# Kernel optimization log

Measured on AMD Instinct MI355X. Metric: run time of the kernel, lower is better.

## Reference

```python
import jax, jax.numpy as jnp
import numpy as np

B, D_IN, J = 65536, 512, 8
HIDDEN = [256, 128, 64]


def setup_inputs() -> dict:
    key = jax.random.key(0)
    ks = jax.random.split(key, 8)
    dims = [D_IN] + HIDDEN
    inp = {
        "x": jax.random.normal(ks[0], (B, D_IN), dtype=jnp.float32),
        # soft domain indicator (one-hot in practice; math is a weighted sum either way)
        "domain_indicator": jax.random.uniform(ks[1], (B, J), dtype=jnp.float32),
    }
    for i in range(3):
        fin, fout = dims[i], dims[i + 1]
        scale = (2.0 / (fin + fout)) ** 0.5  # glorot_normal
        inp[f"sk{i}"] = jax.random.normal(ks[2 + i], (fin, fout), dtype=jnp.float32) * scale
        inp[f"sb{i}"] = jnp.zeros((fout,), dtype=jnp.float32)
        inp[f"dk{i}"] = jax.random.normal(ks[5 + i], (J, fin, fout), dtype=jnp.float32) * scale
        inp[f"db{i}"] = jnp.zeros((J, fout), dtype=jnp.float32)
    return inp


def _star_forward(x, domain_indicator, layers):
    # layer 0: x is [B, D]; fused shared*domain weights -> batched per-domain GEMM
    sk, sb, dk, db = layers[0]
    w = sk[None] * dk                                   # [J, D, H0]
    h = jnp.einsum('bi,jio->bjo', x, w) + (sb[None] + db)[None]  # [B, J, H0]
    h = jax.nn.relu(h)
    for sk, sb, dk, db in layers[1:]:
        w = sk[None] * dk                               # [J, Hi, Hi+1]
        h = jnp.einsum('bji,jio->bjo', h, w) + (sb[None] + db)[None]
        h = jax.nn.relu(h)
    # select/mix domains: sum_j h[b,j,:] * indicator[b,j]
    return jnp.einsum('bjo,bj->bo', h, domain_indicator)


def reference(x, domain_indicator, sk0, sb0, dk0, db0, sk1, sb1, dk1, db1, sk2, sb2, dk2, db2):
    layers = [(sk0, sb0, dk0, db0), (sk1, sb1, dk1, db1), (sk2, sb2, dk2, db2)]
    return _star_forward(x, domain_indicator, layers)
```

## Files before the change

### kernel.cpp

```cpp
#include <hip/hip_runtime.h>
#include <stdint.h>


namespace {

typedef __attribute__((ext_vector_type(8))) short bf16x8;
typedef __attribute__((ext_vector_type(4))) float f32x4;

union Frag { bf16x8 v; unsigned int u[4]; };

constexpr size_t WS_L0   = 0;
constexpr size_t WS_L1   = 4194304;
constexpr size_t WS_L2   = 5242880;
constexpr size_t WS_B0   = 5505024;
constexpr size_t WS_B1   = 5513216;
constexpr size_t WS_B2   = 5517312;
constexpr size_t WS_X    = 5519360;
constexpr size_t WS_TOTAL_BIG = WS_X + (size_t)65536 * 2048;

constexpr int PREP_TOTAL = 1048576 + 262144 + 65536 + 2048 + 1024 + 512;

__device__ __forceinline__ void splitpair(float a, float b,
                                          unsigned int& hi, unsigned int& lo) {
    unsigned int ua = __float_as_uint(a);
    unsigned int ub = __float_as_uint(b);
    unsigned int ha = ua & 0xffff0000u;
    unsigned int hb = ub & 0xffff0000u;
    float ra = a - __uint_as_float(ha);
    float rb = b - __uint_as_float(hb);
    hi = (ua >> 16) | hb;
    lo = (__float_as_uint(ra) >> 16) | (__float_as_uint(rb) & 0xffff0000u);
}

__device__ __forceinline__ void split16(float v, unsigned short& h, unsigned short& l) {
    unsigned int u = __float_as_uint(v);
    h = (unsigned short)(u >> 16);
    float r = v - __uint_as_float(u & 0xffff0000u);
    l = (unsigned short)(__float_as_uint(r) >> 16);
}

__device__ __forceinline__ unsigned int packsplit(float v) {
    unsigned int u = __float_as_uint(v);
    unsigned int h = u & 0xffff0000u;
    float r = v - __uint_as_float(h);
    return h | (__float_as_uint(r) >> 16);
}

__device__ __forceinline__ void unpack2(unsigned int e0, unsigned int e1,
                                        unsigned int& hi, unsigned int& lo) {
    hi = (e0 >> 16) | (e1 & 0xffff0000u);
    lo = (e0 & 0xffffu) | (e1 << 16);
}

__global__ void prep_ws(const float* __restrict__ sk0, const float* __restrict__ dk0,
                        const float* __restrict__ sk1, const float* __restrict__ dk1,
                        const float* __restrict__ sk2, const float* __restrict__ dk2,
                        const float* __restrict__ sb0, const float* __restrict__ db0,
                        const float* __restrict__ sb1, const float* __restrict__ db1,
                        const float* __restrict__ sb2, const float* __restrict__ db2,
                        char* __restrict__ ws) {
    int tid = blockIdx.x * 256 + threadIdx.x;
    if (tid < 1048576) {
        int n = tid & 255, k = (tid >> 8) & 511, j = tid >> 17;
        float wv = sk0[k * 256 + n] * dk0[(size_t)(j * 512 + k) * 256 + n];
        unsigned int u = __float_as_uint(wv);
        unsigned int h = u & 0xffff0000u;
        float r = wv - __uint_as_float(h);
        int pair = (j * 16 + (k >> 5)) * 16 + (n >> 4);
        int lane = (n & 15) | (((k >> 3) & 3) << 4);
        size_t off = WS_L0 + (size_t)pair * 2048 + lane * 16 + (k & 7) * 2;
        *(unsigned short*)(ws + off)        = (unsigned short)(u >> 16);
        *(unsigned short*)(ws + off + 1024) = (unsigned short)(__float_as_uint(r) >> 16);
    } else if (tid < 1310720) {
        int t = tid - 1048576;
        int n = t & 127, k = (t >> 7) & 255, j = t >> 15;
        float wv = sk1[k * 128 + n] * dk1[(size_t)(j * 256 + k) * 128 + n];
        unsigned int u = __float_as_uint(wv);
        unsigned int h = u & 0xffff0000u;
        float r = wv - __uint_as_float(h);
        int pair = (j * 8 + (k >> 5)) * 8 + (n >> 4);
        int lane = (n & 15) | (((k >> 3) & 3) << 4);
        size_t off = WS_L1 + (size_t)pair * 2048 + lane * 16 + (k & 7) * 2;
        *(unsigned short*)(ws + off)        = (unsigned short)(u >> 16);
        *(unsigned short*)(ws + off + 1024) = (unsigned short)(__float_as_uint(r) >> 16);
    } else if (tid < 1376256) {
        int t = tid - 1310720;
        int n = t & 63, k = (t >> 6) & 127, j = t >> 13;
        float wv = sk2[k * 64 + n] * dk2[(size_t)(j * 128 + k) * 64 + n];
        unsigned int u = __float_as_uint(wv);
        unsigned int h = u & 0xffff0000u;
        float r = wv - __uint_as_float(h);
        int pair = (j * 4 + (k >> 5)) * 4 + (n >> 4);
        int lane = (n & 15) | (((k >> 3) & 3) << 4);
        size_t off = WS_L2 + (size_t)pair * 2048 + lane * 16 + (k & 7) * 2;
        *(unsigned short*)(ws + off)        = (unsigned short)(u >> 16);
        *(unsigned short*)(ws + off + 1024) = (unsigned short)(__float_as_uint(r) >> 16);
    } else if (tid < 1378304) {
        int t = tid - 1376256;
        ((float*)(ws + WS_B0))[t] = sb0[t & 255] + db0[t];
    } else if (tid < 1379328) {
        int t = tid - 1378304;
        ((float*)(ws + WS_B1))[t] = sb1[t & 127] + db1[t];
    } else if (tid < PREP_TOTAL) {
        int t = tid - 1379328;
        ((float*)(ws + WS_B2))[t] = sb2[t & 63] + db2[t];
    }
}

__global__ __launch_bounds__(256) void prep_xsplit(const float* __restrict__ x,
                                                   char* __restrict__ ws) {
    __shared__ __align__(16) unsigned int xf[8192];
    const int b     = blockIdx.x;
    const int tid   = threadIdx.x;
    const int row16 = tid >> 4;
    const int seg   = tid & 15;

    const float* src = x + ((size_t)b * 16 + row16) * 512 + seg * 32;
    float4 a[8];
#pragma unroll
    for (int i = 0; i < 8; ++i) a[i] = *(const float4*)(src + i * 4);

    unsigned int hi[16], lo[16];
#pragma unroll
    for (int i = 0; i < 8; ++i) {
        splitpair(a[i].x, a[i].y, hi[2 * i],     lo[2 * i]);
        splitpair(a[i].z, a[i].w, hi[2 * i + 1], lo[2 * i + 1]);
    }
#pragma unroll
    for (int qq = 0; qq < 4; ++qq) {
        const int lane = row16 | (qq << 4);
        const int di = seg * 512 + lane * 4;
        uint4 vh = { hi[qq * 4 + 0], hi[qq * 4 + 1], hi[qq * 4 + 2], hi[qq * 4 + 3] };
        uint4 vl = { lo[qq * 4 + 0], lo[qq * 4 + 1], lo[qq * 4 + 2], lo[qq * 4 + 3] };
        *(uint4*)&xf[di]       = vh;
        *(uint4*)&xf[di + 256] = vl;
    }
    __syncthreads();

    uint4* dst = (uint4*)(ws + WS_X + (size_t)b * 32768) + tid * 8;
#pragma unroll
    for (int i = 0; i < 8; ++i) dst[i] = *(const uint4*)&xf[tid * 32 + i * 4];
}

__global__ __launch_bounds__(512, 4) void star_mfma_v5(
    const float* __restrict__ ind,
    const char* __restrict__ ws,
    float* __restrict__ out)
{
    __shared__ __align__(16) unsigned short H0hi[32 * 264];
    __shared__ __align__(16) unsigned short H0lo[32 * 264];
    __shared__ __align__(16) unsigned short H1hi[32 * 136];
    __shared__ __align__(16) unsigned short H1lo[32 * 136];
    __shared__ float indS[8 * 33];

    const int tid  = threadIdx.x;
    const int w    = tid >> 6;
    const int lane = tid & 63;
    const int c    = lane & 15;
    const int q    = lane >> 4;
    const int b0   = blockIdx.x * 32;
    const int mt2  = w >> 2;
    const int nt2  = w & 3;

    const char* xp  = ws + WS_X;
    const char* wB0 = ws + WS_L0;
    const char* wB1 = ws + WS_L1;
    const char* wB2 = ws + WS_L2;
    const float* bias0 = (const float*)(ws + WS_B0);
    const float* bias1 = (const float*)(ws + WS_B1);
    const float* bias2 = (const float*)(ws + WS_B2);

    if (tid < 256) indS[(tid & 7) * 33 + (tid >> 3)] = ind[(size_t)b0 * 8 + tid];

    const f32x4 z = {0.f, 0.f, 0.f, 0.f};
    f32x4 oacc = z;

    __syncthreads();

    for (int jp = 0; jp < 2; ++jp) {
        f32x4 acc0[4][2][2];
#pragma unroll
        for (int jj = 0; jj < 4; ++jj)
#pragma unroll
            for (int mt = 0; mt < 2; ++mt)
#pragma unroll
                for (int ntl = 0; ntl < 2; ++ntl) acc0[jj][mt][ntl] = z;

        for (int kc = 0; kc < 16; ++kc) {
            Frag Ahi[2], Alo[2];
#pragma unroll
            for (int mt = 0; mt < 2; ++mt) {
                const char* ap = xp + ((size_t)((blockIdx.x * 2 + mt) * 16 + kc) * 2048) + lane * 16;
                *(uint4*)Ahi[mt].u = *(const uint4*)ap;
                *(uint4*)Alo[mt].u = *(const uint4*)(ap + 1024);
            }
#pragma unroll
            for (int jj = 0; jj < 4; ++jj) {
                const int j = jp * 4 + jj;
#pragma unroll
                for (int ntl = 0; ntl < 2; ++ntl) {
                    const int nt = w * 2 + ntl;
                    const char* pb = wB0 + ((size_t)((j * 16 + kc) * 16 + nt) * 2048) + lane * 16;
                    Frag Bhi, Blo;
                    *(uint4*)Bhi.u = *(const uint4*)pb;
                    *(uint4*)Blo.u = *(const uint4*)(pb + 1024);
#pragma unroll
                    for (int mt = 0; mt < 2; ++mt) {
                        acc0[jj][mt][ntl] = __builtin_amdgcn_mfma_f32_16x16x32_bf16(Ahi[mt].v, Bhi.v, acc0[jj][mt][ntl], 0, 0, 0);
                        acc0[jj][mt][ntl] = __builtin_amdgcn_mfma_f32_16x16x32_bf16(Ahi[mt].v, Blo.v, acc0[jj][mt][ntl], 0, 0, 0);
                        acc0[jj][mt][ntl] = __builtin_amdgcn_mfma_f32_16x16x32_bf16(Alo[mt].v, Bhi.v, acc0[jj][mt][ntl], 0, 0, 0);
                    }
                }
            }
        }

#pragma unroll
        for (int jj = 0; jj < 4; ++jj) {
            const int j = jp * 4 + jj;

#pragma unroll
            for (int ntl = 0; ntl < 2; ++ntl) {
                const int k = w * 32 + ntl * 16 + c;
                const float bv = bias0[j * 256 + k];
#pragma unroll
                for (int mt = 0; mt < 2; ++mt)
#pragma unroll
                    for (int r = 0; r < 4; ++r) {
                        float v = fmaxf(acc0[jj][mt][ntl][r] + bv, 0.f);
                        unsigned short h16, l16;
                        split16(v, h16, l16);
                        const int idx = (mt * 16 + q * 4 + r) * 264 + k;
                        H0hi[idx] = h16;
                        H0lo[idx] = l16;
                    }
            }
            __syncthreads();

            f32x4 acc1[2]; acc1[0] = z; acc1[1] = z;
            for (int kc = 0; kc < 8; ++kc) {
                Frag Ahi[2], Alo[2];
#pragma unroll
                for (int mt = 0; mt < 2; ++mt) {
                    const int idx = (mt * 16 + c) * 264 + kc * 32 + q * 8;
                    *(uint4*)Ahi[mt].u = *(const uint4*)&H0hi[idx];
                    *(uint4*)Alo[mt].u = *(const uint4*)&H0lo[idx];
                }
                const char* pb = wB1 + ((size_t)((j * 8 + kc) * 8 + w) * 2048) + lane * 16;
                Frag Bhi, Blo;
                *(uint4*)Bhi.u = *(const uint4*)pb;
                *(uint4*)Blo.u = *(const uint4*)(pb + 1024);
#pragma unroll
                for (int mt = 0; mt < 2; ++mt) {
                    acc1[mt] = __builtin_amdgcn_mfma_f32_16x16x32_bf16(Ahi[mt].v, Bhi.v, acc1[mt], 0, 0, 0);
                    acc1[mt] = __builtin_amdgcn_mfma_f32_16x16x32_bf16(Ahi[mt].v, Blo.v, acc1[mt], 0, 0, 0);
                    acc1[mt] = __builtin_amdgcn_mfma_f32_16x16x32_bf16(Alo[mt].v, Bhi.v, acc1[mt], 0, 0, 0);
                }
            }
            {
                const int k = w * 16 + c;
                const float bv = bias1[j * 128 + k];
#pragma unroll
                for (int mt = 0; mt < 2; ++mt)
#pragma unroll
                    for (int r = 0; r < 4; ++r) {
                        float v = fmaxf(acc1[mt][r] + bv, 0.f);
                        unsigned short h16, l16;
                        split16(v, h16, l16);
                        const int idx = (mt * 16 + q * 4 + r) * 136 + k;
                        H1hi[idx] = h16;
                        H1lo[idx] = l16;
                    }
            }
            __syncthreads();

            f32x4 acc2 = z;
            for (int kc = 0; kc < 4; ++kc) {
                Frag Ahi, Alo;
                const int idx = (mt2 * 16 + c) * 136 + kc * 32 + q * 8;
                *(uint4*)Ahi.u = *(const uint4*)&H1hi[idx];
                *(uint4*)Alo.u = *(const uint4*)&H1lo[idx];
                const char* pb = wB2 + ((size_t)((j * 4 + kc) * 4 + nt2) * 2048) + lane * 16;
                Frag Bhi, Blo;
                *(uint4*)Bhi.u = *(const uint4*)pb;
                *(uint4*)Blo.u = *(const uint4*)(pb + 1024);
                acc2 = __builtin_amdgcn_mfma_f32_16x16x32_bf16(Ahi.v, Bhi.v, acc2, 0, 0, 0);
                acc2 = __builtin_amdgcn_mfma_f32_16x16x32_bf16(Ahi.v, Blo.v, acc2, 0, 0, 0);
                acc2 = __builtin_amdgcn_mfma_f32_16x16x32_bf16(Alo.v, Bhi.v, acc2, 0, 0, 0);
            }
            {
                const float bv = bias2[j * 64 + nt2 * 16 + c];
#pragma unroll
                for (int r = 0; r < 4; ++r) {
                    float v = fmaxf(acc2[r] + bv, 0.f);
                    oacc[r] = fmaf(indS[j * 33 + mt2 * 16 + q * 4 + r], v, oacc[r]);
                }
            }
        }
    }

#pragma unroll
    for (int r = 0; r < 4; ++r)
        out[(size_t)(b0 + mt2 * 16 + q * 4 + r) * 64 + nt2 * 16 + c] = oacc[r];
}

__global__ __launch_bounds__(256, 3) void star_mfma_fb(
    const float* __restrict__ x,
    const float* __restrict__ ind,
    const char* __restrict__ ws,
    float* __restrict__ out)
{
    __shared__ unsigned int H0s[32 * 260];
    __shared__ unsigned int H1s[32 * 132];
    __shared__ float indS[8 * 33];

    const int tid  = threadIdx.x;
    const int w    = tid >> 6;
    const int lane = tid & 63;
    const int c    = lane & 15;
    const int q    = lane >> 4;
    const int b0   = blockIdx.x * 32;

    const char* wB0 = ws + WS_L0;
    const char* wB1 = ws + WS_L1;
    const char* wB2 = ws + WS_L2;
    const float* bias0 = (const float*)(ws + WS_B0);
    const float* bias1 = (const float*)(ws + WS_B1);
    const float* bias2 = (const float*)(ws + WS_B2);

    indS[(tid & 7) * 33 + (tid >> 3)] = ind[(size_t)b0 * 8 + tid];

    const f32x4 z = {0.f, 0.f, 0.f, 0.f};
    f32x4 oacc[2]; oacc[0] = z; oacc[1] = z;

    __syncthreads();

    for (int j = 0; j < 8; ++j) {
        f32x4 acc0[2][4];
#pragma unroll
        for (int mt = 0; mt < 2; ++mt)
#pragma unroll
            for (int ntl = 0; ntl < 4; ++ntl) acc0[mt][ntl] = z;

        for (int kc = 0; kc < 16; ++kc) {
            Frag Ahi[2], Alo[2];
#pragma unroll
            for (int mt = 0; mt < 2; ++mt) {
                const float* ap = x + (size_t)(b0 + mt * 16 + c) * 512 + kc * 32 + q * 8;
                float4 a0 = *(const float4*)ap;
                float4 a1 = *(const float4*)(ap + 4);
                splitpair(a0.x, a0.y, Ahi[mt].u[0], Alo[mt].u[0]);
                splitpair(a0.z, a0.w, Ahi[mt].u[1], Alo[mt].u[1]);
                splitpair(a1.x, a1.y, Ahi[mt].u[2], Alo[mt].u[2]);
                splitpair(a1.z, a1.w, Ahi[mt].u[3], Alo[mt].u[3]);
            }
#pragma unroll
            for (int ntl = 0; ntl < 4; ++ntl) {
                const int nt = w * 4 + ntl;
                const char* pb = wB0 + ((size_t)((j * 16 + kc) * 16 + nt) * 2048) + lane * 16;
                Frag Bhi, Blo;
                *(uint4*)Bhi.u = *(const uint4*)pb;
                *(uint4*)Blo.u = *(const uint4*)(pb + 1024);
#pragma unroll
                for (int mt = 0; mt < 2; ++mt) {
                    acc0[mt][ntl] = __builtin_amdgcn_mfma_f32_16x16x32_bf16(Ahi[mt].v, Bhi.v, acc0[mt][ntl], 0, 0, 0);
                    acc0[mt][ntl] = __builtin_amdgcn_mfma_f32_16x16x32_bf16(Ahi[mt].v, Blo.v, acc0[mt][ntl], 0, 0, 0);
                    acc0[mt][ntl] = __builtin_amdgcn_mfma_f32_16x16x32_bf16(Alo[mt].v, Bhi.v, acc0[mt][ntl], 0, 0, 0);
                }
            }
        }
#pragma unroll
        for (int ntl = 0; ntl < 4; ++ntl) {
            const float bv = bias0[j * 256 + w * 64 + ntl * 16 + c];
#pragma unroll
            for (int mt = 0; mt < 2; ++mt)
#pragma unroll
                for (int r = 0; r < 4; ++r) {
                    float v = acc0[mt][ntl][r] + bv;
                    v = fmaxf(v, 0.f);
                    H0s[(mt * 16 + q * 4 + r) * 260 + w * 64 + ntl * 16 + c] = packsplit(v);
                }
        }
        __syncthreads();

        f32x4 acc1[2][2];
#pragma unroll
        for (int mt = 0; mt < 2; ++mt)
#pragma unroll
            for (int ntl = 0; ntl < 2; ++ntl) acc1[mt][ntl] = z;

        for (int kc = 0; kc < 8; ++kc) {
            Frag Ahi[2], Alo[2];
#pragma unroll
            for (int mt = 0; mt < 2; ++mt) {
                const unsigned int* hp = &H0s[(mt * 16 + c) * 260 + kc * 32 + q * 8];
                uint4 e0 = *(const uint4*)hp;
                uint4 e1 = *(const uint4*)(hp + 4);
                unpack2(e0.x, e0.y, Ahi[mt].u[0], Alo[mt].u[0]);
                unpack2(e0.z, e0.w, Ahi[mt].u[1], Alo[mt].u[1]);
                unpack2(e1.x, e1.y, Ahi[mt].u[2], Alo[mt].u[2]);
                unpack2(e1.z, e1.w, Ahi[mt].u[3], Alo[mt].u[3]);
            }
#pragma unroll
            for (int ntl = 0; ntl < 2; ++ntl) {
                const int nt = w * 2 + ntl;
                const char* pb = wB1 + ((size_t)((j * 8 + kc) * 8 + nt) * 2048) + lane * 16;
                Frag Bhi, Blo;
                *(uint4*)Bhi.u = *(const uint4*)pb;
                *(uint4*)Blo.u = *(const uint4*)(pb + 1024);
#pragma unroll
                for (int mt = 0; mt < 2; ++mt) {
                    acc1[mt][ntl] = __builtin_amdgcn_mfma_f32_16x16x32_bf16(Ahi[mt].v, Bhi.v, acc1[mt][ntl], 0, 0, 0);
                    acc1[mt][ntl] = __builtin_amdgcn_mfma_f32_16x16x32_bf16(Ahi[mt].v, Blo.v, acc1[mt][ntl], 0, 0, 0);
                    acc1[mt][ntl] = __builtin_amdgcn_mfma_f32_16x16x32_bf16(Alo[mt].v, Bhi.v, acc1[mt][ntl], 0, 0, 0);
                }
            }
        }
#pragma unroll
        for (int ntl = 0; ntl < 2; ++ntl) {
            const float bv = bias1[j * 128 + w * 32 + ntl * 16 + c];
#pragma unroll
            for (int mt = 0; mt < 2; ++mt)
#pragma unroll
                for (int r = 0; r < 4; ++r) {
                    float v = acc1[mt][ntl][r] + bv;
                    v = fmaxf(v, 0.f);
                    H1s[(mt * 16 + q * 4 + r) * 132 + w * 32 + ntl * 16 + c] = packsplit(v);
                }
        }
        __syncthreads();

        f32x4 acc2[2]; acc2[0] = z; acc2[1] = z;

        for (int kc = 0; kc < 4; ++kc) {
            Frag Ahi[2], Alo[2];
#pragma unroll
            for (int mt = 0; mt < 2; ++mt) {
                const unsigned int* hp = &H1s[(mt * 16 + c) * 132 + kc * 32 + q * 8];
                uint4 e0 = *(const uint4*)hp;
                uint4 e1 = *(const uint4*)(hp + 4);
                unpack2(e0.x, e0.y, Ahi[mt].u[0], Alo[mt].u[0]);
                unpack2(e0.z, e0.w, Ahi[mt].u[1], Alo[mt].u[1]);
                unpack2(e1.x, e1.y, Ahi[mt].u[2], Alo[mt].u[2]);
                unpack2(e1.z, e1.w, Ahi[mt].u[3], Alo[mt].u[3]);
            }
            const char* pb = wB2 + ((size_t)((j * 4 + kc) * 4 + w) * 2048) + lane * 16;
            Frag Bhi, Blo;
            *(uint4*)Bhi.u = *(const uint4*)pb;
            *(uint4*)Blo.u = *(const uint4*)(pb + 1024);
#pragma unroll
            for (int mt = 0; mt < 2; ++mt) {
                acc2[mt] = __builtin_amdgcn_mfma_f32_16x16x32_bf16(Ahi[mt].v, Bhi.v, acc2[mt], 0, 0, 0);
                acc2[mt] = __builtin_amdgcn_mfma_f32_16x16x32_bf16(Ahi[mt].v, Blo.v, acc2[mt], 0, 0, 0);
                acc2[mt] = __builtin_amdgcn_mfma_f32_16x16x32_bf16(Alo[mt].v, Bhi.v, acc2[mt], 0, 0, 0);
            }
        }
        {
            const float bv = bias2[j * 64 + w * 16 + c];
#pragma unroll
            for (int mt = 0; mt < 2; ++mt)
#pragma unroll
                for (int r = 0; r < 4; ++r) {
                    float v = acc2[mt][r] + bv;
                    v = fmaxf(v, 0.f);
                    oacc[mt][r] = fmaf(indS[j * 33 + mt * 16 + q * 4 + r], v, oacc[mt][r]);
                }
        }
    }

#pragma unroll
    for (int mt = 0; mt < 2; ++mt)
#pragma unroll
        for (int r = 0; r < 4; ++r)
            out[(size_t)(b0 + mt * 16 + q * 4 + r) * 64 + w * 16 + c] = oacc[mt][r];
}

}

extern "C" void kernel_launch(void* const* d_in, const int* in_sizes, int n_in,
                              void* d_out, int out_size, void* d_ws, size_t ws_size,
                              hipStream_t stream) {
    const float* x   = (const float*)d_in[0];
    const float* ind = (const float*)d_in[1];
    const float* sk0 = (const float*)d_in[2];
    const float* sb0 = (const float*)d_in[3];
    const float* dk0 = (const float*)d_in[4];
    const float* db0 = (const float*)d_in[5];
    const float* sk1 = (const float*)d_in[6];
    const float* sb1 = (const float*)d_in[7];
    const float* dk1 = (const float*)d_in[8];
    const float* db1 = (const float*)d_in[9];
    const float* sk2 = (const float*)d_in[10];
    const float* sb2 = (const float*)d_in[11];
    const float* dk2 = (const float*)d_in[12];
    const float* db2 = (const float*)d_in[13];
    char* ws   = (char*)d_ws;
    float* out = (float*)d_out;

    prep_ws<<<dim3((PREP_TOTAL + 255) / 256), dim3(256), 0, stream>>>(
        sk0, dk0, sk1, dk1, sk2, dk2, sb0, db0, sb1, db1, sb2, db2, ws);

    if (ws_size >= WS_TOTAL_BIG) {
        prep_xsplit<<<dim3(4096), dim3(256), 0, stream>>>(x, ws);
        star_mfma_v5<<<dim3(2048), dim3(512), 0, stream>>>(ind, ws, out);
    } else {
        star_mfma_fb<<<dim3(2048), dim3(256), 0, stream>>>(x, ind, ws, out);
    }
}
```

Before: 848.2 us.

## Double batch rows per block to 64 to halve per-domain weight traffic

Measured after the change: 871.8 us. 2.8% more time.

```diff
diff --git a/kernel.cpp b/kernel.cpp
--- a/kernel.cpp
+++ b/kernel.cpp
@@ -142,24 +142,25 @@
     for (int i = 0; i < 8; ++i) dst[i] = *(const uint4*)&xf[tid * 32 + i * 4];
 }
 
-__global__ __launch_bounds__(512, 4) void star_mfma_v5(
+__global__ __launch_bounds__(512, 2) void star_mfma_v6(
     const float* __restrict__ ind,
     const char* __restrict__ ws,
     float* __restrict__ out)
 {
-    __shared__ __align__(16) unsigned short H0hi[32 * 264];
-    __shared__ __align__(16) unsigned short H0lo[32 * 264];
-    __shared__ __align__(16) unsigned short H1hi[32 * 136];
-    __shared__ __align__(16) unsigned short H1lo[32 * 136];
-    __shared__ float indS[8 * 33];
+    __shared__ __align__(16) unsigned short H0hi[64 * 264];
+    __shared__ __align__(16) unsigned short H0lo[64 * 264];
+    __shared__ __align__(16) unsigned short H1hi[64 * 136];
+    __shared__ __align__(16) unsigned short H1lo[64 * 136];
+    __shared__ float indS[8 * 65];
 
     const int tid  = threadIdx.x;
     const int w    = tid >> 6;
     const int lane = tid & 63;
     const int c    = lane & 15;
     const int q    = lane >> 4;
-    const int b0   = blockIdx.x * 32;
-    const int mt2  = w >> 2;
+    const int bx   = blockIdx.x;
+    const int b0   = bx * 64;
+    const int mh   = w >> 2;
     const int nt2  = w & 3;
 
     const char* xp  = ws + WS_X;
@@ -170,27 +171,27 @@
     const float* bias1 = (const float*)(ws + WS_B1);
     const float* bias2 = (const float*)(ws + WS_B2);
 
-    if (tid < 256) indS[(tid & 7) * 33 + (tid >> 3)] = ind[(size_t)b0 * 8 + tid];
+    indS[(tid & 7) * 65 + (tid >> 3)] = ind[(size_t)b0 * 8 + tid];
 
     const f32x4 z = {0.f, 0.f, 0.f, 0.f};
-    f32x4 oacc = z;
+    f32x4 oacc[2]; oacc[0] = z; oacc[1] = z;
 
     __syncthreads();
 
     for (int jp = 0; jp < 2; ++jp) {
-        f32x4 acc0[4][2][2];
+        f32x4 acc0[4][4][2];
 #pragma unroll
         for (int jj = 0; jj < 4; ++jj)
 #pragma unroll
-            for (int mt = 0; mt < 2; ++mt)
+            for (int mt = 0; mt < 4; ++mt)
 #pragma unroll
                 for (int ntl = 0; ntl < 2; ++ntl) acc0[jj][mt][ntl] = z;
 
         for (int kc = 0; kc < 16; ++kc) {
-            Frag Ahi[2], Alo[2];
-#pragma unroll
-            for (int mt = 0; mt < 2; ++mt) {
-                const char* ap = xp + ((size_t)((blockIdx.x * 2 + mt) * 16 + kc) * 2048) + lane * 16;
+            Frag Ahi[4], Alo[4];
+#pragma unroll
+            for (int mt = 0; mt < 4; ++mt) {
+                const char* ap = xp + ((size_t)((bx * 4 + mt) * 16 + kc) * 2048) + lane * 16;
                 *(uint4*)Ahi[mt].u = *(const uint4*)ap;
                 *(uint4*)Alo[mt].u = *(const uint4*)(ap + 1024);
             }
@@ -205,7 +206,7 @@
                     *(uint4*)Bhi.u = *(const uint4*)pb;
                     *(uint4*)Blo.u = *(const uint4*)(pb + 1024);
 #pragma unroll
-                    for (int mt = 0; mt < 2; ++mt) {
+                    for (int mt = 0; mt < 4; ++mt) {
                         acc0[jj][mt][ntl] = __builtin_amdgcn_mfma_f32_16x16x32_bf16(Ahi[mt].v, Bhi.v, acc0[jj][mt][ntl], 0, 0, 0);
                         acc0[jj][mt][ntl] = __builtin_amdgcn_mfma_f32_16x16x32_bf16(Ahi[mt].v, Blo.v, acc0[jj][mt][ntl], 0, 0, 0);
                         acc0[jj][mt][ntl] = __builtin_amdgcn_mfma_f32_16x16x32_bf16(Alo[mt].v, Bhi.v, acc0[jj][mt][ntl], 0, 0, 0);
@@ -223,7 +224,7 @@
                 const int k = w * 32 + ntl * 16 + c;
                 const float bv = bias0[j * 256 + k];
 #pragma unroll
-                for (int mt = 0; mt < 2; ++mt)
+                for (int mt = 0; mt < 4; ++mt)
 #pragma unroll
                     for (int r = 0; r < 4; ++r) {
                         float v = fmaxf(acc0[jj][mt][ntl][r] + bv, 0.f);
@@ -236,11 +237,13 @@
             }
             __syncthreads();
 
-            f32x4 acc1[2]; acc1[0] = z; acc1[1] = z;
+            f32x4 acc1[4];
+#pragma unroll
+            for (int mt = 0; mt < 4; ++mt) acc1[mt] = z;
             for (int kc = 0; kc < 8; ++kc) {
-                Frag Ahi[2], Alo[2];
-#pragma unroll
-                for (int mt = 0; mt < 2; ++mt) {
+                Frag Ahi[4], Alo[4];
+#pragma unroll
+                for (int mt = 0; mt < 4; ++mt) {
                     const int idx = (mt * 16 + c) * 264 + kc * 32 + q * 8;
                     *(uint4*)Ahi[mt].u = *(const uint4*)&H0hi[idx];
                     *(uint4*)Alo[mt].u = *(const uint4*)&H0lo[idx];
@@ -250,7 +253,7 @@
                 *(uint4*)Bhi.u = *(const uint4*)pb;
                 *(uint4*)Blo.u = *(const uint4*)(pb + 1024);
 #pragma unroll
-                for (int mt = 0; mt < 2; ++mt) {
+                for (int mt = 0; mt < 4; ++mt) {
                     acc1[mt] = __builtin_amdgcn_mfma_f32_16x16x32_bf16(Ahi[mt].v, Bhi.v, acc1[mt], 0, 0, 0);
                     acc1[mt] = __builtin_amdgcn_mfma_f32_16x16x32_bf16(Ahi[mt].v, Blo.v, acc1[mt], 0, 0, 0);
                     acc1[mt] = __builtin_amdgcn_mfma_f32_16x16x32_bf16(Alo[mt].v, Bhi.v, acc1[mt], 0, 0, 0);
@@ -260,7 +263,7 @@
                 const int k = w * 16 + c;
                 const float bv = bias1[j * 128 + k];
 #pragma unroll
-                for (int mt = 0; mt < 2; ++mt)
+                for (int mt = 0; mt < 4; ++mt)
 #pragma unroll
                     for (int r = 0; r < 4; ++r) {
                         float v = fmaxf(acc1[mt][r] + bv, 0.f);
@@ -273,34 +276,42 @@
             }
             __syncthreads();
 
-            f32x4 acc2 = z;
+            f32x4 acc2[2]; acc2[0] = z; acc2[1] = z;
             for (int kc = 0; kc < 4; ++kc) {
-                Frag Ahi, Alo;
-                const int idx = (mt2 * 16 + c) * 136 + kc * 32 + q * 8;
-                *(uint4*)Ahi.u = *(const uint4*)&H1hi[idx];
-                *(uint4*)Alo.u = *(const uint4*)&H1lo[idx];
                 const char* pb = wB2 + ((size_t)((j * 4 + kc) * 4 + nt2) * 2048) + lane * 16;
                 Frag Bhi, Blo;
                 *(uint4*)Bhi.u = *(const uint4*)pb;
                 *(uint4*)Blo.u = *(const uint4*)(pb + 1024);
-                acc2 = __builtin_amdgcn_mfma_f32_16x16x32_bf16(Ahi.v, Bhi.v, acc2, 0, 0, 0);
-                acc2 = __builtin_amdgcn_mfma_f32_16x16x32_bf16(Ahi.v, Blo.v, acc2, 0, 0, 0);
-                acc2 = __builtin_amdgcn_mfma_f32_16x16x32_bf16(Alo.v, Bhi.v, acc2, 0, 0, 0);
+#pragma unroll
+                for (int mtl = 0; mtl < 2; ++mtl) {
+                    Frag Ahi, Alo;
+                    const int idx = ((mh * 2 + mtl) * 16 + c) * 136 + kc * 32 + q * 8;
+                    *(uint4*)Ahi.u = *(const uint4*)&H1hi[idx];
+                    *(uint4*)Alo.u = *(const uint4*)&H1lo[idx];
+                    acc2[mtl] = __builtin_amdgcn_mfma_f32_16x16x32_bf16(Ahi.v, Bhi.v, acc2[mtl], 0, 0, 0);
+                    acc2[mtl] = __builtin_amdgcn_mfma_f32_16x16x32_bf16(Ahi.v, Blo.v, acc2[mtl], 0, 0, 0);
+                    acc2[mtl] = __builtin_amdgcn_mfma_f32_16x16x32_bf16(Alo.v, Bhi.v, acc2[mtl], 0, 0, 0);
+                }
             }
             {
                 const float bv = bias2[j * 64 + nt2 * 16 + c];
 #pragma unroll
-                for (int r = 0; r < 4; ++r) {
-                    float v = fmaxf(acc2[r] + bv, 0.f);
-                    oacc[r] = fmaf(indS[j * 33 + mt2 * 16 + q * 4 + r], v, oacc[r]);
-                }
+                for (int mtl = 0; mtl < 2; ++mtl)
+#pragma unroll
+                    for (int r = 0; r < 4; ++r) {
+                        float v = fmaxf(acc2[mtl][r] + bv, 0.f);
+                        const int m = (mh * 2 + mtl) * 16 + q * 4 + r;
+                        oacc[mtl][r] = fmaf(indS[j * 65 + m], v, oacc[mtl][r]);
+                    }
             }
         }
     }
 
 #pragma unroll
-    for (int r = 0; r < 4; ++r)
-        out[(size_t)(b0 + mt2 * 16 + q * 4 + r) * 64 + nt2 * 16 + c] = oacc[r];
+    for (int mtl = 0; mtl < 2; ++mtl)
+#pragma unroll
+        for (int r = 0; r < 4; ++r)
+            out[(size_t)(b0 + (mh * 2 + mtl) * 16 + q * 4 + r) * 64 + nt2 * 16 + c] = oacc[mtl][r];
 }
 
 __global__ __launch_bounds__(256, 3) void star_mfma_fb(
@@ -501,7 +512,7 @@
 
     if (ws_size >= WS_TOTAL_BIG) {
         prep_xsplit<<<dim3(4096), dim3(256), 0, stream>>>(x, ws);
-        star_mfma_v5<<<dim3(2048), dim3(512), 0, stream>>>(ind, ws, out);
+        star_mfma_v6<<<dim3(1024), dim3(512), 0, stream>>>(ind, ws, out);
     } else {
         star_mfma_fb<<<dim3(2048), dim3(256), 0, stream>>>(x, ind, ws, out);
     }
```
